# Optimization experiments

Hardware: AMD Instinct MI355X
Metric: run time of the kernel (lower is better)

Reference implementation:

```python
import jax, jax.numpy as jnp
import numpy as np

C = 256          # feature channels (forced by 256*7*7 MLP input)
FS = 7           # gaussian filter size
G = 8            # RoIAlignAvg samples an (P+1)x(P+1) grid then 2x2 avg-pools
POOL = 7         # cfg.POOLING_SIZE
SCALE = 1.0 / 16.0
NK = 12          # 3 ratios * 4 scales
B, H, W, R = 2, 64, 64, 128
HID = 4096
IN_DIM = C * POOL * POOL


def _make_kernels():
    """Replicates gaussian_kernel() from __init__ for every anchor size."""
    ratios = [0.5, 1.0, 2.0]
    scales = [4, 8, 16, 32]
    sizes = []
    for s in scales:
        area = (s * 16) ** 2
        for r in ratios:
            sizes.append(((r * area) ** 0.5, (area / r) ** 0.5))  # (h, w)
    K = np.zeros((NK, C, 1, FS, FS), np.float32)
    c = FS // 2
    idx = np.arange(FS, dtype=np.float32)
    for k, (h, w) in enumerate(sizes):
        x_sigma = w / (7.0 * 16.0)  # scale*(x2-x1)/(bins*stride), roi=(0,0,0,w,h)
        y_sigma = h / (7.0 * 16.0)
        xr = (idx - c) ** 2 / x_sigma ** 2
        yr = (idx - c) ** 2 / y_sigma ** 2
        K[k, :, 0] = np.exp(-(yr[:, None] + xr[None, :]) / 2.0)
    return jnp.asarray(K)


def _roi_align(feat, rois5):
    """RoIAlignAvg: bilinear crop to 8x8 grid (corners on roi corners), then
    2x2 stride-1 average pool -> 7x7. feat: [B,C,H,W], rois5: [N,5]."""
    Hf, Wf = feat.shape[2], feat.shape[3]
    grid = jnp.arange(G, dtype=feat.dtype) / (G - 1)

    def one(roi):
        b = roi[0].astype(jnp.int32)
        img = jnp.take(feat, b, axis=0)  # [C,H,W]
        x1, y1, x2, y2 = roi[1] * SCALE, roi[2] * SCALE, roi[3] * SCALE, roi[4] * SCALE
        xs = jnp.clip(x1 + (x2 - x1) * grid, 0.0, Wf - 1)
        ys = jnp.clip(y1 + (y2 - y1) * grid, 0.0, Hf - 1)
        x0f = jnp.floor(xs); wx = xs - x0f
        y0f = jnp.floor(ys); wy = ys - y0f
        x0 = x0f.astype(jnp.int32); x1i = jnp.minimum(x0 + 1, Wf - 1)
        y0 = y0f.astype(jnp.int32); y1i = jnp.minimum(y0 + 1, Hf - 1)
        g = lambda yi, xi: img[:, yi[:, None], xi[None, :]]  # [C,G,G]
        top = g(y0, x0) * (1 - wx) + g(y0, x1i) * wx
        bot = g(y1i, x0) * (1 - wx) + g(y1i, x1i) * wx
        crop = top * (1 - wy)[:, None] + bot * wy[:, None]  # [C,G,G]
        return 0.25 * (crop[:, :-1, :-1] + crop[:, 1:, :-1]
                       + crop[:, :-1, 1:] + crop[:, 1:, 1:])  # [C,7,7]

    return jax.vmap(one)(rois5)


def setup_inputs() -> dict:
    key = jax.random.key(0)
    ks = jax.random.split(key, 8)
    base_feat = jax.random.normal(ks[0], (B, C, H, W), jnp.float32)
    kernel = _make_kernels()
    N = B * R
    bidx = jnp.repeat(jnp.arange(B, dtype=jnp.float32), R)
    x1 = jax.random.uniform(ks[1], (N,), minval=0.0, maxval=760.0)
    y1 = jax.random.uniform(ks[2], (N,), minval=0.0, maxval=760.0)
    bw = jax.random.uniform(ks[3], (N,), minval=64.0, maxval=256.0)
    bh = jax.random.uniform(ks[4], (N,), minval=64.0, maxval=256.0)
    x2 = jnp.minimum(x1 + bw, 1023.0)
    y2 = jnp.minimum(y1 + bh, 1023.0)
    rois = jnp.stack([bidx, x1, y1, x2, y2], axis=1).reshape(B, R, 5)
    W1 = jax.random.normal(ks[5], (HID, IN_DIM), jnp.float32) * 0.01
    b1 = jnp.zeros((HID,), jnp.float32)
    g1 = jnp.ones((HID,), jnp.float32); be1 = jnp.zeros((HID,), jnp.float32)
    m1 = jnp.zeros((HID,), jnp.float32); v1 = jnp.ones((HID,), jnp.float32)
    W2 = jax.random.normal(ks[6], (NK, HID), jnp.float32) * 0.01
    b2 = jnp.zeros((NK,), jnp.float32)
    g2 = jnp.ones((NK,), jnp.float32); be2 = jnp.zeros((NK,), jnp.float32)
    m2 = jnp.zeros((NK,), jnp.float32); v2 = jnp.ones((NK,), jnp.float32)
    return dict(base_feat=base_feat, kernel=kernel, rois=rois,
                W1=W1, b1=b1, g1=g1, be1=be1, m1=m1, v1=v1,
                W2=W2, b2=b2, g2=g2, be2=be2, m2=m2, v2=v2)


def reference(base_feat, kernel, rois, W1, b1, g1, be1, m1, v1,
              W2, b2, g2, be2, m2, v2):
    eps = 1e-5
    pad = FS // 2
    dw = lambda k: jax.lax.conv_general_dilated(
        base_feat, k, (1, 1), [(pad, pad), (pad, pad)],
        dimension_numbers=('NCHW', 'OIHW', 'NCHW'), feature_group_count=C)
    filtered = jnp.stack([dw(kernel[i]) for i in range(NK)], 0)  # [NK,B,C,H,W]
    r5 = rois.reshape(-1, 5)
    pooled = _roi_align(base_feat, r5)                            # [N,C,7,7]
    pooled_list = jax.vmap(lambda f: _roi_align(f, r5))(filtered)  # [NK,N,C,7,7]
    x = pooled.reshape(pooled.shape[0], -1)                       # [N, C*7*7]
    h = x @ W1.T + b1
    h = (h - m1) * jax.lax.rsqrt(v1 + eps) * g1 + be1
    h = jax.nn.relu(h)
    o = h @ W2.T + b2
    o = (o - m2) * jax.lax.rsqrt(v2 + eps) * g2 + be2
    wgt = jax.nn.softmax(o, axis=1).T.reshape(NK, -1, 1, 1, 1)    # [NK,N,1,1,1]
    return jnp.sum(pooled_list * wgt, axis=0)                     # [N,C,7,7]
```

## Files before the change

kernel.cpp:

```cpp
#include <hip/hip_runtime.h>

#define NB    2
#define NC    256
#define NH    64
#define NW    64
#define PADW  72
#define NKF   12
#define NROI  256
#define HID   4096
#define INDIM 12544
#define KCH   8
#define KCLEN 1568

typedef __attribute__((ext_vector_type(8))) short short8;
typedef __attribute__((ext_vector_type(4))) float floatx4;

__device__ __forceinline__ unsigned short f2bf(float f) {
  unsigned int u = __float_as_uint(f);
  u += 0x7fffu + ((u >> 16) & 1u);
  return (unsigned short)(u >> 16);
}

__global__ void k_transpose(const float* __restrict__ base, float* __restrict__ featT,
                            unsigned short* __restrict__ featB) {
  int bid = blockIdx.x;
  int b = bid >> 6, y = bid & 63;
  __shared__ float tile[64][65];
  for (int cc = 0; cc < 4; ++cc) {
    int c0 = cc * 64;
    #pragma unroll
    for (int i = 0; i < 16; ++i) {
      int idx = threadIdx.x + i * 256;
      int ci = idx >> 6, xi = idx & 63;
      tile[ci][xi] = base[(((b * NC) + c0 + ci) * NH + y) * NW + xi];
    }
    __syncthreads();
    #pragma unroll
    for (int i = 0; i < 16; ++i) {
      int idx = threadIdx.x + i * 256;
      int xo = idx >> 6, co = idx & 63;
      float v = tile[co][xo];
      size_t o = (((size_t)b * PADW + y + 3) * PADW + xo + 3) * NC + c0 + co;
      featT[o] = v;
      featB[o] = f2bf(v);
    }
    __syncthreads();
  }
}

template<int GY0, int GYN, int P0, int PN, int GX0, int GXN, int Q0, int QN>
__device__ __forceinline__ void roi_base_quad(const float* __restrict__ featT,
                                              const float* __restrict__ rois,
                                              unsigned short* __restrict__ xbf,
                                              int n, int c) {
  const float* r = rois + n * 5;
  int b = (int)r[0];
  float x1 = r[1] * 0.0625f, y1 = r[2] * 0.0625f;
  float x2 = r[3] * 0.0625f, y2 = r[4] * 0.0625f;
  int ix0[GXN], ix1[GXN], iy0[GYN], iy1[GYN];
  float wx[GXN], wy[GYN];
  #pragma unroll
  for (int i = 0; i < GXN; ++i) {
    float xs = fminf(fmaxf(x1 + (x2 - x1) * ((GX0 + i) * (1.f / 7.f)), 0.f), 63.f);
    float xf = floorf(xs);
    ix0[i] = (int)xf; ix1[i] = min(ix0[i] + 1, 63); wx[i] = xs - xf;
  }
  #pragma unroll
  for (int i = 0; i < GYN; ++i) {
    float ys = fminf(fmaxf(y1 + (y2 - y1) * ((GY0 + i) * (1.f / 7.f)), 0.f), 63.f);
    float yf = floorf(ys);
    iy0[i] = (int)yf; iy1[i] = min(iy0[i] + 1, 63); wy[i] = ys - yf;
  }
  const float* fb = featT + ((size_t)b * (PADW * PADW) + 3 * PADW + 3) * NC + c;
  float cg[GYN][GXN];
  #pragma unroll
  for (int gy = 0; gy < GYN; ++gy) {
    int r0 = iy0[gy] * (PADW * NC), r1 = iy1[gy] * (PADW * NC);
    #pragma unroll
    for (int gx = 0; gx < GXN; ++gx) {
      int c0 = ix0[gx] * NC, c1 = ix1[gx] * NC;
      float v00 = fb[r0 + c0], v01 = fb[r0 + c1];
      float v10 = fb[r1 + c0], v11 = fb[r1 + c1];
      float top = v00 + (v01 - v00) * wx[gx];
      float bot = v10 + (v11 - v10) * wx[gx];
      cg[gy][gx] = top + (bot - top) * wy[gy];
    }
  }
  unsigned short* xp = xbf + (size_t)n * INDIM + c * 49;
  #pragma unroll
  for (int p = P0; p < P0 + PN; ++p)
    #pragma unroll
    for (int q = Q0; q < Q0 + QN; ++q)
      xp[p * 7 + q] = f2bf(0.25f * (cg[p - GY0][q - GX0] + cg[p - GY0][q - GX0 + 1]
                                    + cg[p - GY0 + 1][q - GX0] + cg[p - GY0 + 1][q - GX0 + 1]));
}

__global__ void __launch_bounds__(256) k_roi_base(const float* __restrict__ featT,
                                                  const float* __restrict__ rois,
                                                  unsigned short* __restrict__ xbf) {
  int n = blockIdx.x, qd = blockIdx.y, c = threadIdx.x;
  switch (qd) {
    case 0: roi_base_quad<0, 4, 0, 3, 0, 4, 0, 3>(featT, rois, xbf, n, c); break;
    case 1: roi_base_quad<0, 4, 0, 3, 3, 5, 3, 4>(featT, rois, xbf, n, c); break;
    case 2: roi_base_quad<3, 5, 3, 4, 0, 4, 0, 3>(featT, rois, xbf, n, c); break;
    default: roi_base_quad<3, 5, 3, 4, 3, 5, 3, 4>(featT, rois, xbf, n, c); break;
  }
}

__global__ void __launch_bounds__(256) k_gemm1(const unsigned short* __restrict__ A,
                                               const float* __restrict__ W1,
                                               float* __restrict__ partial) {
  __shared__ unsigned short As[256 * 40];
  __shared__ unsigned short Bs[64 * 40];
  int nb = blockIdx.x, kc = blockIdx.y;
  int j0 = nb * 64;
  int kbase = kc * KCLEN;
  int tid = threadIdx.x;
  int wv = tid >> 6, lane = tid & 63;
  int quad = lane >> 4, l15 = lane & 15;
  int m0 = wv * 64;
  floatx4 acc[4][4];
  #pragma unroll
  for (int i = 0; i < 4; ++i)
    #pragma unroll
    for (int j = 0; j < 4; ++j) acc[i][j] = (floatx4)0.0f;

  for (int ks = 0; ks < KCLEN / 32; ++ks) {
    int kk = kbase + ks * 32;
    #pragma unroll
    for (int rr = 0; rr < 4; ++rr) {
      int q = tid + rr * 256;
      int row = q >> 2, part = q & 3;
      short8 av = *(const short8*)(A + (size_t)row * INDIM + kk + part * 8);
      *(short8*)(As + row * 40 + part * 8) = av;
    }
    #pragma unroll
    for (int rr = 0; rr < 2; ++rr) {
      int q = tid + rr * 256;
      int row = q >> 3, part = q & 7;
      floatx4 bv = *(const floatx4*)(W1 + (size_t)(j0 + row) * INDIM + kk + part * 4);
      union { unsigned short us[4]; unsigned long long u; } cv;
      cv.us[0] = f2bf(bv.x); cv.us[1] = f2bf(bv.y);
      cv.us[2] = f2bf(bv.z); cv.us[3] = f2bf(bv.w);
      *(unsigned long long*)(Bs + row * 40 + part * 4) = cv.u;
    }
    __syncthreads();
    short8 af[4];
    #pragma unroll
    for (int mi = 0; mi < 4; ++mi)
      af[mi] = *(const short8*)(As + (m0 + mi * 16 + l15) * 40 + quad * 8);
    #pragma unroll
    for (int ni = 0; ni < 4; ++ni) {
      short8 bfv = *(const short8*)(Bs + (ni * 16 + l15) * 40 + quad * 8);
      #pragma unroll
      for (int mi = 0; mi < 4; ++mi)
        acc[mi][ni] = __builtin_amdgcn_mfma_f32_16x16x32_bf16(af[mi], bfv, acc[mi][ni], 0, 0, 0);
    }
    __syncthreads();
  }
  float* po = partial + (size_t)kc * (NROI * HID);
  #pragma unroll
  for (int mi = 0; mi < 4; ++mi) {
    #pragma unroll
    for (int ni = 0; ni < 4; ++ni) {
      int j = j0 + ni * 16 + l15;
      #pragma unroll
      for (int rg = 0; rg < 4; ++rg) {
        int m = m0 + mi * 16 + quad * 4 + rg;
        po[(size_t)m * HID + j] = acc[mi][ni][rg];
      }
    }
  }
}

__global__ void __launch_bounds__(256) k_reduce_head(
    const float* __restrict__ partial,
    const float* __restrict__ b1, const float* __restrict__ g1,
    const float* __restrict__ be1, const float* __restrict__ m1,
    const float* __restrict__ v1, const float* __restrict__ W2,
    const float* __restrict__ b2, const float* __restrict__ g2,
    const float* __restrict__ be2, const float* __restrict__ m2,
    const float* __restrict__ v2, float* __restrict__ wgt) {
  int n = blockIdx.x, tid = threadIdx.x;
  float p[NKF];
  #pragma unroll
  for (int k = 0; k < NKF; ++k) p[k] = 0.f;
  #pragma unroll 4
  for (int jj = 0; jj < HID / 256; ++jj) {
    int j = jj * 256 + tid;
    float s = 0.f;
    #pragma unroll
    for (int kc = 0; kc < KCH; ++kc)
      s += partial[(size_t)kc * (NROI * HID) + (size_t)n * HID + j];
    s += b1[j];
    s = (s - m1[j]) * rsqrtf(v1[j] + 1e-5f) * g1[j] + be1[j];
    s = fmaxf(s, 0.f);
    #pragma unroll
    for (int k = 0; k < NKF; ++k) p[k] += s * W2[k * HID + j];
  }
  #pragma unroll
  for (int k = 0; k < NKF; ++k) {
    #pragma unroll
    for (int off = 32; off > 0; off >>= 1) p[k] += __shfl_down(p[k], off, 64);
  }
  __shared__ float red[4][NKF];
  int wv = tid >> 6, lane = tid & 63;
  if (lane == 0) {
    #pragma unroll
    for (int k = 0; k < NKF; ++k) red[wv][k] = p[k];
  }
  __syncthreads();
  if (tid == 0) {
    float o[NKF], mx = -1e30f;
    #pragma unroll
    for (int k = 0; k < NKF; ++k) {
      float t = red[0][k] + red[1][k] + red[2][k] + red[3][k] + b2[k];
      t = (t - m2[k]) * rsqrtf(v2[k] + 1e-5f) * g2[k] + be2[k];
      o[k] = t;
      mx = fmaxf(mx, t);
    }
    float s = 0.f;
    #pragma unroll
    for (int k = 0; k < NKF; ++k) { o[k] = __expf(o[k] - mx); s += o[k]; }
    float inv = 1.f / s;
    #pragma unroll
    for (int k = 0; k < NKF; ++k) wgt[n * NKF + k] = o[k] * inv;
  }
}

__global__ void __launch_bounds__(256, 1) k_final(const unsigned short* __restrict__ featB,
                                                  const float* __restrict__ rois,
                                                  const float* __restrict__ wgt,
                                                  const float* __restrict__ kern,
                                                  float* __restrict__ out) {
  __shared__ __align__(16) unsigned short win[24 * 24 * 64];
  __shared__ float bmk[64 * 65];
  __shared__ __align__(16) float S[64 * 68];
  __shared__ float swx[64], swy[64], mk[49];
  __shared__ int srel[64], sw0[2];

  int n = blockIdx.x, c0 = blockIdx.y * 64;
  int tid = threadIdx.x;
  const float* r = rois + n * 5;
  int b = (int)r[0];

  if (tid < 64) {
    int gy = tid >> 3, gx = tid & 7;
    float x1 = r[1] * 0.0625f, y1 = r[2] * 0.0625f;
    float x2 = r[3] * 0.0625f, y2 = r[4] * 0.0625f;
    float xs = fminf(fmaxf(x1 + (x2 - x1) * (gx * (1.f / 7.f)), 0.f), 63.f);
    float ys = fminf(fmaxf(y1 + (y2 - y1) * (gy * (1.f / 7.f)), 0.f), 63.f);
    float xf = floorf(xs), yf = floorf(ys);
    int x0 = (int)xf, y0 = (int)yf;
    swx[tid] = xs - xf; swy[tid] = ys - yf;
    int mnx = x0, mny = y0;
    #pragma unroll
    for (int m = 1; m < 64; m <<= 1) {
      mnx = min(mnx, __shfl_xor(mnx, m, 64));
      mny = min(mny, __shfl_xor(mny, m, 64));
    }
    srel[tid] = (y0 - mny) * 24 + (x0 - mnx);
    if (tid == 0) { sw0[0] = mnx; sw0[1] = mny; }
  } else if (tid >= 64 && tid < 64 + 49) {
    int t = tid - 64;
    float m = 0.f;
    #pragma unroll
    for (int k = 0; k < NKF; ++k)
      m += wgt[n * NKF + k] * kern[k * (NC * 49) + t];
    mk[t] = m;
  }
  __syncthreads();
  int wx0 = sw0[0], wy0 = sw0[1];

  const unsigned short* fb = featB + (size_t)b * (PADW * PADW * NC) + c0;
  #pragma unroll
  for (int it = 0; it < 18; ++it) {
    int idx = tid + it * 256;
    int ch8 = idx & 7;
    int cell = idx >> 3;
    int col = cell % 24, row = cell / 24;
    int gr = wy0 + row, gc = wx0 + col;
    if (gr < PADW && gc < PADW) {
      short8 v = *(const short8*)(fb + ((size_t)gr * PADW + gc) * NC + ch8 * 8);
      *(short8*)(win + cell * 64 + ch8 * 8) = v;
    }
  }
  #pragma unroll
  for (int it = 0; it < 16; ++it) {
    int idx = tid + it * 256;
    int s = idx >> 6, e = idx & 63, i = e >> 3, j = e & 7;
    float wxs = swx[s], wys = swy[s];
    float w00 = (1.f - wys) * (1.f - wxs), w01 = (1.f - wys) * wxs;
    float w10 = wys * (1.f - wxs),         w11 = wys * wxs;
    float v = 0.f;
    if (i < 7 && j < 7)   v += w00 * mk[i * 7 + j];
    if (i < 7 && j >= 1)  v += w01 * mk[i * 7 + j - 1];
    if (i >= 1 && j < 7)  v += w10 * mk[(i - 1) * 7 + j];
    if (i >= 1 && j >= 1) v += w11 * mk[(i - 1) * 7 + j - 1];
    bmk[s * 65 + e] = v;
  }
  __syncthreads();

  int c4 = (tid & 15) * 4, sg = tid >> 4;
  #pragma unroll
  for (int t = 0; t < 4; ++t) {
    int s = sg * 4 + t;
    int base = srel[s];
    const float* bw = bmk + s * 65;
    float a0 = 0.f, a1 = 0.f, a2 = 0.f, a3 = 0.f;
    #pragma unroll
    for (int i = 0; i < 8; ++i) {
      #pragma unroll
      for (int j = 0; j < 8; ++j) {
        float w = bw[i * 8 + j];
        uint2 u = *(const uint2*)(win + (base + i * 24 + j) * 64 + c4);
        float v0 = __uint_as_float(u.x << 16);
        float v1 = __uint_as_float(u.x & 0xffff0000u);
        float v2 = __uint_as_float(u.y << 16);
        float v3 = __uint_as_float(u.y & 0xffff0000u);
        a0 += w * v0; a1 += w * v1; a2 += w * v2; a3 += w * v3;
      }
    }
    floatx4 res; res.x = a0; res.y = a1; res.z = a2; res.w = a3;
    *(floatx4*)(S + s * 68 + c4) = res;
  }
  __syncthreads();

  for (int it = 0; it < 13; ++it) {
    int idx = tid + it * 256;
    if (idx >= 64 * 49) break;
    int c = idx / 49, pq = idx % 49;
    int p = pq / 7, q = pq % 7;
    int s00 = p * 8 + q;
    float val = 0.25f * (S[s00 * 68 + c] + S[(s00 + 1) * 68 + c]
                         + S[(s00 + 8) * 68 + c] + S[(s00 + 9) * 68 + c]);
    out[((size_t)n * NC + c0 + c) * 49 + pq] = val;
  }
}

extern "C" void kernel_launch(void* const* d_in, const int* in_sizes, int n_in,
                              void* d_out, int out_size, void* d_ws, size_t ws_size,
                              hipStream_t stream) {
  const float* base = (const float*)d_in[0];
  const float* kern = (const float*)d_in[1];
  const float* rois = (const float*)d_in[2];
  const float* W1  = (const float*)d_in[3];
  const float* b1  = (const float*)d_in[4];
  const float* g1  = (const float*)d_in[5];
  const float* be1 = (const float*)d_in[6];
  const float* m1  = (const float*)d_in[7];
  const float* v1  = (const float*)d_in[8];
  const float* W2  = (const float*)d_in[9];
  const float* b2  = (const float*)d_in[10];
  const float* g2  = (const float*)d_in[11];
  const float* be2 = (const float*)d_in[12];
  const float* m2  = (const float*)d_in[13];
  const float* v2  = (const float*)d_in[14];
  float* out = (float*)d_out;

  char* ws = (char*)d_ws;
  const size_t FEATT_BYTES = (size_t)NB * PADW * PADW * NC * 4;
  const size_t FEATB_BYTES = (size_t)NB * PADW * PADW * NC * 2;
  float*          featT   = (float*)(ws);
  unsigned short* featB   = (unsigned short*)(ws + 10616832);
  unsigned short* xbf     = (unsigned short*)(ws + 15925248);
  float*          partial = (float*)(ws + 22347776);
  float*          wgt     = (float*)(ws + 55902208);

  hipMemsetAsync(featT, 0, FEATT_BYTES, stream);
  hipMemsetAsync(featB, 0, FEATB_BYTES, stream);
  hipLaunchKernelGGL(k_transpose, dim3(NB * NH), dim3(256), 0, stream, base, featT, featB);
  hipLaunchKernelGGL(k_roi_base, dim3(NROI, 4), dim3(256), 0, stream, featT, rois, xbf);
  hipLaunchKernelGGL(k_gemm1, dim3(64, KCH), dim3(256), 0, stream, xbf, W1, partial);
  hipLaunchKernelGGL(k_reduce_head, dim3(NROI), dim3(256), 0, stream,
                     partial, b1, g1, be1, m1, v1, W2, b2, g2, be2, m2, v2, wgt);
  hipLaunchKernelGGL(k_final, dim3(NROI, 4), dim3(256), 0, stream, featB, rois, wgt, kern, out);
}
```

Measured before the change: 506.7 us.

## Drop fp32 feature copy and memsets, prefetch GEMM tiles, split final kernel finer

```diff
diff --git a/kernel.cpp b/kernel.cpp
--- a/kernel.cpp
+++ b/kernel.cpp
@@ -20,36 +20,53 @@
   u += 0x7fffu + ((u >> 16) & 1u);
   return (unsigned short)(u >> 16);
 }
-
-__global__ void k_transpose(const float* __restrict__ base, float* __restrict__ featT,
+__device__ __forceinline__ float bf2f(unsigned short s) {
+  return __uint_as_float(((unsigned int)s) << 16);
+}
+
+__global__ void k_transpose(const float* __restrict__ base,
                             unsigned short* __restrict__ featB) {
   int bid = blockIdx.x;
   int b = bid >> 6, y = bid & 63;
+  int tid = threadIdx.x;
   __shared__ float tile[64][65];
   for (int cc = 0; cc < 4; ++cc) {
     int c0 = cc * 64;
     #pragma unroll
     for (int i = 0; i < 16; ++i) {
-      int idx = threadIdx.x + i * 256;
+      int idx = tid + i * 256;
       int ci = idx >> 6, xi = idx & 63;
       tile[ci][xi] = base[(((b * NC) + c0 + ci) * NH + y) * NW + xi];
     }
     __syncthreads();
     #pragma unroll
-    for (int i = 0; i < 16; ++i) {
-      int idx = threadIdx.x + i * 256;
-      int xo = idx >> 6, co = idx & 63;
-      float v = tile[co][xo];
-      size_t o = (((size_t)b * PADW + y + 3) * PADW + xo + 3) * NC + c0 + co;
-      featT[o] = v;
-      featB[o] = f2bf(v);
+    for (int i = 0; i < 8; ++i) {
+      int idx = tid + i * 256;
+      int xo = idx >> 5, cp = idx & 31;
+      unsigned int lo = f2bf(tile[cp * 2][xo]);
+      unsigned int hi = f2bf(tile[cp * 2 + 1][xo]);
+      unsigned int pack = lo | (hi << 16);
+      size_t o = (((size_t)b * PADW + y + 3) * PADW + xo + 3) * NC + c0 + cp * 2;
+      *(unsigned int*)(featB + o) = pack;
     }
     __syncthreads();
   }
+  int hb = bid & 63;
+  unsigned int* fz = (unsigned int*)(featB + (size_t)b * (PADW * PADW * NC));
+  #pragma unroll
+  for (int t = 0; t < 17; ++t) {
+    int hidx = hb * 17 + t;
+    int r, c;
+    if (hidx < 216)       { r = hidx / 72;            c = hidx % 72; }
+    else if (hidx < 576)  { int j = hidx - 216; r = 67 + j / 72; c = j % 72; }
+    else                  { int j = hidx - 576; r = 3 + (j >> 3);
+                            int k = j & 7; c = (k < 3) ? k : (64 + k); }
+    if (tid < 128) fz[((size_t)r * PADW + c) * (NC / 2) + tid] = 0u;
+  }
 }
 
 template<int GY0, int GYN, int P0, int PN, int GX0, int GXN, int Q0, int QN>
-__device__ __forceinline__ void roi_base_quad(const float* __restrict__ featT,
+__device__ __forceinline__ void roi_base_quad(const unsigned short* __restrict__ featB,
                                               const float* __restrict__ rois,
                                               unsigned short* __restrict__ xbf,
                                               int n, int c) {
@@ -71,7 +88,7 @@
     float yf = floorf(ys);
     iy0[i] = (int)yf; iy1[i] = min(iy0[i] + 1, 63); wy[i] = ys - yf;
   }
-  const float* fb = featT + ((size_t)b * (PADW * PADW) + 3 * PADW + 3) * NC + c;
+  const unsigned short* fb = featB + ((size_t)b * (PADW * PADW) + 3 * PADW + 3) * NC + c;
   float cg[GYN][GXN];
   #pragma unroll
   for (int gy = 0; gy < GYN; ++gy) {
@@ -79,8 +96,8 @@
     #pragma unroll
     for (int gx = 0; gx < GXN; ++gx) {
       int c0 = ix0[gx] * NC, c1 = ix1[gx] * NC;
-      float v00 = fb[r0 + c0], v01 = fb[r0 + c1];
-      float v10 = fb[r1 + c0], v11 = fb[r1 + c1];
+      float v00 = bf2f(fb[r0 + c0]), v01 = bf2f(fb[r0 + c1]);
+      float v10 = bf2f(fb[r1 + c0]), v11 = bf2f(fb[r1 + c1]);
       float top = v00 + (v01 - v00) * wx[gx];
       float bot = v10 + (v11 - v10) * wx[gx];
       cg[gy][gx] = top + (bot - top) * wy[gy];
@@ -95,15 +112,15 @@
                                     + cg[p - GY0 + 1][q - GX0] + cg[p - GY0 + 1][q - GX0 + 1]));
 }
 
-__global__ void __launch_bounds__(256) k_roi_base(const float* __restrict__ featT,
+__global__ void __launch_bounds__(256) k_roi_base(const unsigned short* __restrict__ featB,
                                                   const float* __restrict__ rois,
                                                   unsigned short* __restrict__ xbf) {
   int n = blockIdx.x, qd = blockIdx.y, c = threadIdx.x;
   switch (qd) {
-    case 0: roi_base_quad<0, 4, 0, 3, 0, 4, 0, 3>(featT, rois, xbf, n, c); break;
-    case 1: roi_base_quad<0, 4, 0, 3, 3, 5, 3, 4>(featT, rois, xbf, n, c); break;
-    case 2: roi_base_quad<3, 5, 3, 4, 0, 4, 0, 3>(featT, rois, xbf, n, c); break;
-    default: roi_base_quad<3, 5, 3, 4, 3, 5, 3, 4>(featT, rois, xbf, n, c); break;
+    case 0: roi_base_quad<0, 4, 0, 3, 0, 4, 0, 3>(featB, rois, xbf, n, c); break;
+    case 1: roi_base_quad<0, 4, 0, 3, 3, 5, 3, 4>(featB, rois, xbf, n, c); break;
+    case 2: roi_base_quad<3, 5, 3, 4, 0, 4, 0, 3>(featB, rois, xbf, n, c); break;
+    default: roi_base_quad<3, 5, 3, 4, 3, 5, 3, 4>(featB, rois, xbf, n, c); break;
   }
 }
 
@@ -125,26 +142,39 @@
     #pragma unroll
     for (int j = 0; j < 4; ++j) acc[i][j] = (floatx4)0.0f;
 
+  int arow = tid >> 2, apart = tid & 3;
+  int brow = tid >> 3, bpart = tid & 7;
+  const unsigned short* aptr = A + (size_t)arow * INDIM + kbase + apart * 8;
+  const float* bptr = W1 + (size_t)(j0 + brow) * INDIM + kbase + bpart * 4;
+
+  short8 avP[4];
+  floatx4 bvP[2];
+  #pragma unroll
+  for (int rr = 0; rr < 4; ++rr) avP[rr] = *(const short8*)(aptr + (size_t)rr * 64 * INDIM);
+  #pragma unroll
+  for (int rr = 0; rr < 2; ++rr) bvP[rr] = *(const floatx4*)(bptr + (size_t)rr * 32 * INDIM);
+
   for (int ks = 0; ks < KCLEN / 32; ++ks) {
-    int kk = kbase + ks * 32;
-    #pragma unroll
-    for (int rr = 0; rr < 4; ++rr) {
-      int q = tid + rr * 256;
-      int row = q >> 2, part = q & 3;
-      short8 av = *(const short8*)(A + (size_t)row * INDIM + kk + part * 8);
-      *(short8*)(As + row * 40 + part * 8) = av;
-    }
+    #pragma unroll
+    for (int rr = 0; rr < 4; ++rr)
+      *(short8*)(As + (arow + rr * 64) * 40 + apart * 8) = avP[rr];
     #pragma unroll
     for (int rr = 0; rr < 2; ++rr) {
-      int q = tid + rr * 256;
-      int row = q >> 3, part = q & 7;
-      floatx4 bv = *(const floatx4*)(W1 + (size_t)(j0 + row) * INDIM + kk + part * 4);
       union { unsigned short us[4]; unsigned long long u; } cv;
-      cv.us[0] = f2bf(bv.x); cv.us[1] = f2bf(bv.y);
-      cv.us[2] = f2bf(bv.z); cv.us[3] = f2bf(bv.w);
-      *(unsigned long long*)(Bs + row * 40 + part * 4) = cv.u;
+      cv.us[0] = f2bf(bvP[rr].x); cv.us[1] = f2bf(bvP[rr].y);
+      cv.us[2] = f2bf(bvP[rr].z); cv.us[3] = f2bf(bvP[rr].w);
+      *(unsigned long long*)(Bs + (brow + rr * 32) * 40 + bpart * 4) = cv.u;
     }
     __syncthreads();
+    if (ks < KCLEN / 32 - 1) {
+      int off = (ks + 1) * 32;
+      #pragma unroll
+      for (int rr = 0; rr < 4; ++rr)
+        avP[rr] = *(const short8*)(aptr + (size_t)rr * 64 * INDIM + off);
+      #pragma unroll
+      for (int rr = 0; rr < 2; ++rr)
+        bvP[rr] = *(const floatx4*)(bptr + (size_t)rr * 32 * INDIM + off);
+    }
     short8 af[4];
     #pragma unroll
     for (int mi = 0; mi < 4; ++mi)
@@ -228,18 +258,18 @@
   }
 }
 
-__global__ void __launch_bounds__(256, 1) k_final(const unsigned short* __restrict__ featB,
+__global__ void __launch_bounds__(256, 2) k_final(const unsigned short* __restrict__ featB,
                                                   const float* __restrict__ rois,
                                                   const float* __restrict__ wgt,
                                                   const float* __restrict__ kern,
                                                   float* __restrict__ out) {
-  __shared__ __align__(16) unsigned short win[24 * 24 * 64];
+  __shared__ __align__(16) unsigned short win[576 * 40];
   __shared__ float bmk[64 * 65];
-  __shared__ __align__(16) float S[64 * 68];
+  __shared__ __align__(16) float S[64 * 36];
   __shared__ float swx[64], swy[64], mk[49];
   __shared__ int srel[64], sw0[2];
 
-  int n = blockIdx.x, c0 = blockIdx.y * 64;
+  int n = blockIdx.x, c0 = blockIdx.y * 32;
   int tid = threadIdx.x;
   const float* r = rois + n * 5;
   int b = (int)r[0];
@@ -274,15 +304,15 @@
 
   const unsigned short* fb = featB + (size_t)b * (PADW * PADW * NC) + c0;
   #pragma unroll
-  for (int it = 0; it < 18; ++it) {
+  for (int it = 0; it < 9; ++it) {
     int idx = tid + it * 256;
-    int ch8 = idx & 7;
-    int cell = idx >> 3;
+    int g = idx & 3;
+    int cell = idx >> 2;
     int col = cell % 24, row = cell / 24;
     int gr = wy0 + row, gc = wx0 + col;
     if (gr < PADW && gc < PADW) {
-      short8 v = *(const short8*)(fb + ((size_t)gr * PADW + gc) * NC + ch8 * 8);
-      *(short8*)(win + cell * 64 + ch8 * 8) = v;
+      short8 v = *(const short8*)(fb + ((size_t)gr * PADW + gc) * NC + g * 8);
+      *(short8*)(win + cell * 40 + g * 8) = v;
     }
   }
   #pragma unroll
@@ -301,40 +331,46 @@
   }
   __syncthreads();
 
-  int c4 = (tid & 15) * 4, sg = tid >> 4;
-  #pragma unroll
-  for (int t = 0; t < 4; ++t) {
-    int s = sg * 4 + t;
+  {
+    int s = tid >> 2, g = tid & 3;
     int base = srel[s];
     const float* bw = bmk + s * 65;
     float a0 = 0.f, a1 = 0.f, a2 = 0.f, a3 = 0.f;
+    float a4 = 0.f, a5 = 0.f, a6 = 0.f, a7 = 0.f;
     #pragma unroll
     for (int i = 0; i < 8; ++i) {
       #pragma unroll
       for (int j = 0; j < 8; ++j) {
         float w = bw[i * 8 + j];
-        uint2 u = *(const uint2*)(win + (base + i * 24 + j) * 64 + c4);
-        float v0 = __uint_as_float(u.x << 16);
-        float v1 = __uint_as_float(u.x & 0xffff0000u);
-        float v2 = __uint_as_float(u.y << 16);
-        float v3 = __uint_as_float(u.y & 0xffff0000u);
-        a0 += w * v0; a1 += w * v1; a2 += w * v2; a3 += w * v3;
+        uint4 u = *(const uint4*)(win + (base + i * 24 + j) * 40 + g * 8);
+        a0 += w * __uint_as_float(u.x << 16);
+        a1 += w * __uint_as_float(u.x & 0xffff0000u);
+        a2 += w * __uint_as_float(u.y << 16);
+        a3 += w * __uint_as_float(u.y & 0xffff0000u);
+        a4 += w * __uint_as_float(u.z << 16);
+        a5 += w * __uint_as_float(u.z & 0xffff0000u);
+        a6 += w * __uint_as_float(u.w << 16);
+        a7 += w * __uint_as_float(u.w & 0xffff0000u);
       }
     }
-    floatx4 res; res.x = a0; res.y = a1; res.z = a2; res.w = a3;
-    *(floatx4*)(S + s * 68 + c4) = res;
+    floatx4 r0; r0.x = a0; r0.y = a1; r0.z = a2; r0.w = a3;
+    floatx4 r1; r1.x = a4; r1.y = a5; r1.z = a6; r1.w = a7;
+    *(floatx4*)(S + s * 36 + g * 8) = r0;
+    *(floatx4*)(S + s * 36 + g * 8 + 4) = r1;
   }
   __syncthreads();
 
-  for (int it = 0; it < 13; ++it) {
+  #pragma unroll
+  for (int it = 0; it < 7; ++it) {
     int idx = tid + it * 256;
-    if (idx >= 64 * 49) break;
-    int c = idx / 49, pq = idx % 49;
-    int p = pq / 7, q = pq % 7;
-    int s00 = p * 8 + q;
-    float val = 0.25f * (S[s00 * 68 + c] + S[(s00 + 1) * 68 + c]
-                         + S[(s00 + 8) * 68 + c] + S[(s00 + 9) * 68 + c]);
-    out[((size_t)n * NC + c0 + c) * 49 + pq] = val;
+    if (idx < 32 * 49) {
+      int c = idx / 49, pq = idx % 49;
+      int p = pq / 7, q = pq % 7;
+      int s00 = p * 8 + q;
+      float val = 0.25f * (S[s00 * 36 + c] + S[(s00 + 1) * 36 + c]
+                           + S[(s00 + 8) * 36 + c] + S[(s00 + 9) * 36 + c]);
+      out[((size_t)n * NC + c0 + c) * 49 + pq] = val;
+    }
   }
 }
 
@@ -359,20 +395,15 @@
   float* out = (float*)d_out;
 
   char* ws = (char*)d_ws;
-  const size_t FEATT_BYTES = (size_t)NB * PADW * PADW * NC * 4;
-  const size_t FEATB_BYTES = (size_t)NB * PADW * PADW * NC * 2;
-  float*          featT   = (float*)(ws);
-  unsigned short* featB   = (unsigned short*)(ws + 10616832);
-  unsigned short* xbf     = (unsigned short*)(ws + 15925248);
-  float*          partial = (float*)(ws + 22347776);
-  float*          wgt     = (float*)(ws + 55902208);
-
-  hipMemsetAsync(featT, 0, FEATT_BYTES, stream);
-  hipMemsetAsync(featB, 0, FEATB_BYTES, stream);
-  hipLaunchKernelGGL(k_transpose, dim3(NB * NH), dim3(256), 0, stream, base, featT, featB);
-  hipLaunchKernelGGL(k_roi_base, dim3(NROI, 4), dim3(256), 0, stream, featT, rois, xbf);
+  unsigned short* featB   = (unsigned short*)(ws);
+  unsigned short* xbf     = (unsigned short*)(ws + 5308416);
+  float*          partial = (float*)(ws + 11730944);
+  float*          wgt     = (float*)(ws + 45285376);
+
+  hipLaunchKernelGGL(k_transpose, dim3(NB * NH), dim3(256), 0, stream, base, featB);
+  hipLaunchKernelGGL(k_roi_base, dim3(NROI, 4), dim3(256), 0, stream, featB, rois, xbf);
   hipLaunchKernelGGL(k_gemm1, dim3(64, KCH), dim3(256), 0, stream, xbf, W1, partial);
   hipLaunchKernelGGL(k_reduce_head, dim3(NROI), dim3(256), 0, stream,
                      partial, b1, g1, be1, m1, v1, W2, b2, g2, be2, m2, v2, wgt);
-  hipLaunchKernelGGL(k_final, dim3(NROI, 4), dim3(256), 0, stream, featB, rois, wgt, kern, out);
-}
+  hipLaunchKernelGGL(k_final, dim3(NROI, 8), dim3(256), 0, stream, featB, rois, wgt, kern, out);
+}
```

After: 488.6 us. 3.6% less time.
